# Kernel optimization log

Hardware: AMD Instinct MI355X
Metric: run time of the kernel (lower is better)

Reference implementation:

```python
import jax, jax.numpy as jnp
import numpy as np

B, C, D, K = 256, 512, 1024, 16

def setup_inputs() -> dict:
    key = jax.random.key(0)
    k1, k2 = jax.random.split(key)
    inputs = jax.random.normal(k1, (B, C, D), dtype=jnp.float32)
    W = jax.random.normal(k2, (1, D), dtype=jnp.float32) * (1.0 / np.sqrt(D))
    b = jnp.zeros((1,), dtype=jnp.float32)
    return {"inputs": inputs, "W": W, "b": b, "topk": K}

def reference(inputs, W, b, topk):
    # energy: [B, C] = Linear(inputs) squeezed; softmax over clips
    energy = jnp.einsum('bcd,d->bc', inputs, W[0]) + b[0]
    attn = jax.nn.softmax(energy, axis=1)
    # top-k clip indices by attention weight (descending, like torch.topk)
    _, idx = jax.lax.top_k(attn, topk)          # [B, K]
    # gather the selected clips: [B, K, D]
    selected = jnp.take_along_axis(inputs, idx[:, :, None], axis=1)
    return selected
```

## Files before the change

### kernel.cpp

```cpp
#include <hip/hip_runtime.h>
#include <math.h>

#define NB 256
#define NC 512
#define ND 1024
#define NK 16

__global__ __launch_bounds__(256) void energy_kernel(
    const float4* __restrict__ in,
    const float4* __restrict__ W,
    float* __restrict__ energy)
{
    const int row  = blockIdx.x * 4 + (threadIdx.x >> 6);
    const int lane = threadIdx.x & 63;

    const float4* r = in + (size_t)row * (ND / 4);

    float acc = 0.f;
#pragma unroll
    for (int j = 0; j < 4; ++j) {
        float4 a = r[lane + j * 64];
        float4 w = W[lane + j * 64];
        acc += a.x * w.x + a.y * w.y + a.z * w.z + a.w * w.w;
    }

#pragma unroll
    for (int off = 32; off; off >>= 1)
        acc += __shfl_down(acc, off, 64);

    if (lane == 0) energy[row] = acc;
}

__global__ __launch_bounds__(256) void topk_gather_kernel(
    const float* __restrict__ energy,
    const float4* __restrict__ in,
    float4* __restrict__ out)
{
    const int b   = blockIdx.x;
    const int tid = threadIdx.x;

    __shared__ float e[NC];
    __shared__ int   topidx[NK];
    __shared__ float wv[4];
    __shared__ int   wi[4];

    e[tid]       = energy[b * NC + tid];
    e[tid + 256] = energy[b * NC + tid + 256];
    __syncthreads();

    for (int k = 0; k < NK; ++k) {
        float v0 = e[tid], v1 = e[tid + 256];
        float bv;
        int   bi;
        if (v1 > v0) { bv = v1; bi = tid + 256; }
        else         { bv = v0; bi = tid; }

#pragma unroll
        for (int off = 32; off; off >>= 1) {
            float ov = __shfl_down(bv, off, 64);
            int   oi = __shfl_down(bi, off, 64);
            if (ov > bv || (ov == bv && oi < bi)) { bv = ov; bi = oi; }
        }

        const int lane = tid & 63;
        const int w    = tid >> 6;
        if (lane == 0) { wv[w] = bv; wi[w] = bi; }
        __syncthreads();

        if (tid == 0) {
            float fv = wv[0];
            int   fi = wi[0];
#pragma unroll
            for (int j = 1; j < 4; ++j)
                if (wv[j] > fv || (wv[j] == fv && wi[j] < fi)) { fv = wv[j]; fi = wi[j]; }
            topidx[k] = fi;
            e[fi] = -INFINITY;
        }
        __syncthreads();
    }

#pragma unroll 4
    for (int k = 0; k < NK; ++k) {
        const int c = topidx[k];
        const float4* src = in  + ((size_t)b * NC + c) * (ND / 4);
        float4*       dst = out + ((size_t)b * NK + k) * (ND / 4);
        dst[tid] = src[tid];
    }
}

extern "C" void kernel_launch(void* const* d_in, const int* in_sizes, int n_in,
                              void* d_out, int out_size, void* d_ws, size_t ws_size,
                              hipStream_t stream)
{
    const float* in = (const float*)d_in[0];
    const float* W  = (const float*)d_in[1];

    float* out    = (float*)d_out;
    float* energy = (float*)d_ws;

    energy_kernel<<<NB * NC / 4, 256, 0, stream>>>(
        (const float4*)in, (const float4*)W, energy);

    topk_gather_kernel<<<NB, 256, 0, stream>>>(
        energy, (const float4*)in, (float4*)out);
}
```

Before: 690.2 us.

## Fuse energy, top-k and gather into one per-batch kernel

Merges the dot-product energy pass, top-k selection and row gather into a single kernel with one 1024-thread block per batch. Energies stay in shared memory instead of a workspace round trip. Top-k runs in one wave with per-lane register candidates and no block-wide barriers per iteration. The trade-off is lower occupancy (one block per batch) for the bandwidth-bound energy pass, and ties within a lane's candidates pick the lowest index only implicitly.

```diff
diff --git a/kernel.cpp b/kernel.cpp
--- a/kernel.cpp
+++ b/kernel.cpp
@@ -6,85 +6,92 @@
 #define ND 1024
 #define NK 16
 
-__global__ __launch_bounds__(256) void energy_kernel(
+__global__ __launch_bounds__(1024) void EnergyAttention_fused_kernel(
     const float4* __restrict__ in,
-    const float4* __restrict__ W,
-    float* __restrict__ energy)
-{
-    const int row  = blockIdx.x * 4 + (threadIdx.x >> 6);
-    const int lane = threadIdx.x & 63;
-
-    const float4* r = in + (size_t)row * (ND / 4);
-
-    float acc = 0.f;
-#pragma unroll
-    for (int j = 0; j < 4; ++j) {
-        float4 a = r[lane + j * 64];
-        float4 w = W[lane + j * 64];
-        acc += a.x * w.x + a.y * w.y + a.z * w.z + a.w * w.w;
-    }
-
-#pragma unroll
-    for (int off = 32; off; off >>= 1)
-        acc += __shfl_down(acc, off, 64);
-
-    if (lane == 0) energy[row] = acc;
-}
-
-__global__ __launch_bounds__(256) void topk_gather_kernel(
-    const float* __restrict__ energy,
-    const float4* __restrict__ in,
+    const float4* __restrict__ W4,
     float4* __restrict__ out)
 {
-    const int b   = blockIdx.x;
-    const int tid = threadIdx.x;
+    const int b    = blockIdx.x;
+    const int tid  = threadIdx.x;
+    const int wave = tid >> 6;
+    const int lane = tid & 63;
 
     __shared__ float e[NC];
     __shared__ int   topidx[NK];
-    __shared__ float wv[4];
-    __shared__ int   wi[4];
 
-    e[tid]       = energy[b * NC + tid];
-    e[tid + 256] = energy[b * NC + tid + 256];
-    __syncthreads();
+    const float4 w0 = W4[lane];
+    const float4 w1 = W4[lane + 64];
+    const float4 w2 = W4[lane + 128];
+    const float4 w3 = W4[lane + 192];
 
-    for (int k = 0; k < NK; ++k) {
-        float v0 = e[tid], v1 = e[tid + 256];
-        float bv;
-        int   bi;
-        if (v1 > v0) { bv = v1; bi = tid + 256; }
-        else         { bv = v0; bi = tid; }
+    const float4* base = in + (size_t)b * NC * (ND / 4);
+
+    for (int r = 0; r < 32; r += 2) {
+        const int c0 = wave * 32 + r;
+        const float4* r0 = base + (size_t)c0 * (ND / 4);
+        const float4* r1 = r0 + (ND / 4);
+
+        float4 a0 = r0[lane], b0 = r0[lane + 64], c0v = r0[lane + 128], d0 = r0[lane + 192];
+        float4 a1 = r1[lane], b1 = r1[lane + 64], c1v = r1[lane + 128], d1 = r1[lane + 192];
+
+        float acc0 = 0.f, acc1 = 0.f;
+        acc0 += a0.x * w0.x + a0.y * w0.y + a0.z * w0.z + a0.w * w0.w;
+        acc0 += b0.x * w1.x + b0.y * w1.y + b0.z * w1.z + b0.w * w1.w;
+        acc0 += c0v.x * w2.x + c0v.y * w2.y + c0v.z * w2.z + c0v.w * w2.w;
+        acc0 += d0.x * w3.x + d0.y * w3.y + d0.z * w3.z + d0.w * w3.w;
+
+        acc1 += a1.x * w0.x + a1.y * w0.y + a1.z * w0.z + a1.w * w0.w;
+        acc1 += b1.x * w1.x + b1.y * w1.y + b1.z * w1.z + b1.w * w1.w;
+        acc1 += c1v.x * w2.x + c1v.y * w2.y + c1v.z * w2.z + c1v.w * w2.w;
+        acc1 += d1.x * w3.x + d1.y * w3.y + d1.z * w3.z + d1.w * w3.w;
 
 #pragma unroll
         for (int off = 32; off; off >>= 1) {
-            float ov = __shfl_down(bv, off, 64);
-            int   oi = __shfl_down(bi, off, 64);
-            if (ov > bv || (ov == bv && oi < bi)) { bv = ov; bi = oi; }
+            acc0 += __shfl_down(acc0, off, 64);
+            acc1 += __shfl_down(acc1, off, 64);
         }
+        if (lane == 0) { e[c0] = acc0; e[c0 + 1] = acc1; }
+    }
+    __syncthreads();
 
-        const int lane = tid & 63;
-        const int w    = tid >> 6;
-        if (lane == 0) { wv[w] = bv; wi[w] = bi; }
-        __syncthreads();
+    if (wave == 0) {
+        const int idxbase = lane * 8;
+        float v[8];
+#pragma unroll
+        for (int j = 0; j < 8; ++j) v[j] = e[idxbase + j];
 
-        if (tid == 0) {
-            float fv = wv[0];
-            int   fi = wi[0];
+        for (int k = 0; k < NK; ++k) {
+            float bv = v[0];
+            int   bj = 0;
 #pragma unroll
-            for (int j = 1; j < 4; ++j)
-                if (wv[j] > fv || (wv[j] == fv && wi[j] < fi)) { fv = wv[j]; fi = wi[j]; }
-            topidx[k] = fi;
-            e[fi] = -INFINITY;
+            for (int j = 1; j < 8; ++j)
+                if (v[j] > bv) { bv = v[j]; bj = j; }
+            int bi = idxbase + bj;
+
+#pragma unroll
+            for (int off = 32; off; off >>= 1) {
+                float ov = __shfl_down(bv, off, 64);
+                int   oi = __shfl_down(bi, off, 64);
+                if (ov > bv || (ov == bv && oi < bi)) { bv = ov; bi = oi; }
+            }
+
+            const int win = __shfl(bi, 0, 64);
+            if (lane == 0) topidx[k] = win;
+
+#pragma unroll
+            for (int j = 0; j < 8; ++j)
+                if (win == idxbase + j) v[j] = -INFINITY;
         }
-        __syncthreads();
     }
+    __syncthreads();
 
-#pragma unroll 4
-    for (int k = 0; k < NK; ++k) {
-        const int c = topidx[k];
-        const float4* src = in  + ((size_t)b * NC + c) * (ND / 4);
-        float4*       dst = out + ((size_t)b * NK + k) * (ND / 4);
-        dst[tid] = src[tid];
+    const int g = tid >> 8;
+    const int t = tid & 255;
+#pragma unroll
+    for (int k = 0; k < NK / 4; ++k) {
+        const int kk = k * 4 + g;
+        const int c  = topidx[kk];
+        out[((size_t)b * NK + kk) * (ND / 4) + t] = base[(size_t)c * (ND / 4) + t];
     }
 }
 
@@ -95,12 +102,8 @@
     const float* in = (const float*)d_in[0];
     const float* W  = (const float*)d_in[1];
 
-    float* out    = (float*)d_out;
-    float* energy = (float*)d_ws;
+    float* out = (float*)d_out;
 
-    energy_kernel<<<NB * NC / 4, 256, 0, stream>>>(
-        (const float4*)in, (const float4*)W, energy);
-
-    topk_gather_kernel<<<NB, 256, 0, stream>>>(
-        energy, (const float4*)in, (float4*)out);
+    EnergyAttention_fused_kernel<<<NB, 1024, 0, stream>>>(
+        (const float4*)in, (const float4*)W, (float4*)out);
 }
```

Result: no change. 685.5 us (-0.7%).
